# Kernel optimization log

Hardware: AMD Instinct MI355X
Metric: run time of the kernel (lower is better)

## Reference

```python
import jax, jax.numpy as jnp
import numpy as np

K = 20
EPS = 1e-5


def knn_idx(x, k):
    # x: (B,C,N); returns indices of k nearest neighbors (largest negative sq dist)
    xx = jnp.sum(x * x, axis=1)                       # (B,N)
    inner = jnp.einsum('bcn,bcm->bnm', x, x)          # (B,N,N)
    dist = 2.0 * inner - xx[:, :, None] - xx[:, None, :]
    return jax.lax.top_k(dist, k)[1]                  # (B,N,k)


def gather_nb(x, idx):
    # x: (B,C,N), idx: (B,N,k) -> (B,N,k,C)
    xt = jnp.transpose(x, (0, 2, 1))
    return jax.vmap(lambda t, i: t[i])(xt, idx)


def bn(x, g, b, m, v):
    # eval-mode batchnorm over channel axis 1
    sh = [1] * x.ndim
    sh[1] = -1
    inv = g / jnp.sqrt(v + EPS)
    return (x - m.reshape(sh)) * inv.reshape(sh) + b.reshape(sh)


def graph_feature(x, k=K):
    # x: (B,C,N) -> (B,3C,N,k): [neighbor, center, center-neighbor]
    idx = knn_idx(x, k)
    nb = gather_nb(x, idx)                            # (B,N,k,C)
    ctr = jnp.broadcast_to(jnp.transpose(x, (0, 2, 1))[:, :, None, :], nb.shape)
    f = jnp.concatenate([nb, ctr, ctr - nb], axis=-1)
    return jnp.transpose(f, (0, 3, 1, 2))


def att_pool(x, g, b, m, v, W, wb):
    # x: (B,C,N,k); BN->ReLU->1x1 conv -> softmax over k -> weighted sum
    h = jax.nn.relu(bn(x, g, b, m, v))
    act = jnp.einsum('bcnk,oc->bonk', h, W) + wb[None, :, None, None]
    scores = jax.nn.softmax(act, axis=-1)
    return jnp.sum(x * scores, axis=-1)               # (B,C,N)


def lafe(x, W1, b1, W2, b2, W3, b3):
    # local attention extraction; x: (B,3,N) -> (B,16,N)
    idx = knn_idx(x, K)
    nb = gather_nb(x, idx)                            # (B,N,k,3)
    ctr = jnp.broadcast_to(jnp.transpose(x, (0, 2, 1))[:, :, None, :], nb.shape)
    x_n = ctr - nb
    new_f = jnp.einsum('bnkc,oc->bnko', ctr, W1) + b1
    self_att = jnp.einsum('bnko,o->bnk', new_f, W3[0]) + b3[0]
    edge = jnp.einsum('bnkc,oc->bnko', x_n, W2) + b2  # (B,N,k,16)
    nb_att = jnp.einsum('bnko,o->bnk', edge, W3[0]) + b3[0]
    logits = self_att + nb_att                        # (B,N,k)
    coefs = jax.nn.softmax(jax.nn.leaky_relu(logits, 0.01), axis=-1)
    vals = jnp.einsum('bnk,bnko->bno', coefs, edge)   # (B,N,16)
    return jnp.transpose(jax.nn.elu(vals), (0, 2, 1))


def _forward(x, law1, lab1, law2, lab2, law3, lab3,
             mlp_w, mlp_b, mlp_g, mlp_be, mlp_m, mlp_v,
             c1_w, bn1_g, bn1_b, bn1_m, bn1_v,
             p1_g, p1_b, p1_m, p1_v, p1_w, p1_wb,
             c2_w, bn2_g, bn2_b, bn2_m, bn2_v,
             p2_g, p2_b, p2_m, p2_v, p2_w, p2_wb,
             c3_w, bn3_g, bn3_b, bn3_m, bn3_v):
    xm = lafe(x, law1, lab1, law2, lab2, law3, lab3)          # (B,16,N)
    x_manet = jnp.concatenate([x, xm], axis=1)                # (B,19,N)
    x_mlp = jax.nn.relu(bn(jnp.einsum('bcn,oc->bon', x_manet, mlp_w) + mlp_b[None, :, None],
                           mlp_g, mlp_be, mlp_m, mlp_v))      # (B,256,N)
    g = graph_feature(x_manet)                                # (B,57,N,k)
    h1 = jax.nn.leaky_relu(bn(jnp.einsum('bcnk,oc->bonk', g, c1_w),
                              bn1_g, bn1_b, bn1_m, bn1_v), 0.2)
    x_p1 = att_pool(h1, p1_g, p1_b, p1_m, p1_v, p1_w, p1_wb)  # (B,64,N)
    x_c1 = jnp.concatenate([x_manet, x_p1], axis=1)           # (B,83,N)
    g2 = graph_feature(x_c1)                                  # (B,249,N,k)
    h2 = jax.nn.leaky_relu(bn(jnp.einsum('bcnk,oc->bonk', g2, c2_w),
                              bn2_g, bn2_b, bn2_m, bn2_v), 0.2)
    x_p2 = att_pool(h2, p2_g, p2_b, p2_m, p2_v, p2_w, p2_wb)  # (B,256,N)
    x_c2 = jnp.concatenate([x_mlp, x_p2], axis=1)             # (B,512,N)
    return jax.nn.leaky_relu(bn(jnp.einsum('bcn,oc->bon', x_c2, c3_w),
                                bn3_g, bn3_b, bn3_m, bn3_v), 0.2)


def setup_inputs() -> dict:
    key = jax.random.key(0)
    ks = iter(jax.random.split(key, 16))
    f32 = jnp.float32
    def W(*s):
        return jax.random.normal(next(ks), s, f32) * 0.05
    B, N = 8, 2048
    def bn_params(c):
        return jnp.ones((c,), f32), jnp.zeros((c,), f32), jnp.zeros((c,), f32), jnp.ones((c,), f32)
    d = {}
    d['x'] = jax.random.normal(next(ks), (B, 3, N), f32)
    d['law1'], d['lab1'] = W(16, 3), jnp.zeros((16,), f32)
    d['law2'], d['lab2'] = W(16, 3), jnp.zeros((16,), f32)
    d['law3'], d['lab3'] = W(1, 16), jnp.zeros((1,), f32)
    d['mlp_w'], d['mlp_b'] = W(256, 19), jnp.zeros((256,), f32)
    d['mlp_g'], d['mlp_be'], d['mlp_m'], d['mlp_v'] = bn_params(256)
    d['c1_w'] = W(64, 57)
    d['bn1_g'], d['bn1_b'], d['bn1_m'], d['bn1_v'] = bn_params(64)
    d['p1_g'], d['p1_b'], d['p1_m'], d['p1_v'] = bn_params(64)
    d['p1_w'], d['p1_wb'] = W(64, 64), jnp.zeros((64,), f32)
    d['c2_w'] = W(256, 249)
    d['bn2_g'], d['bn2_b'], d['bn2_m'], d['bn2_v'] = bn_params(256)
    d['p2_g'], d['p2_b'], d['p2_m'], d['p2_v'] = bn_params(256)
    d['p2_w'], d['p2_wb'] = W(256, 256), jnp.zeros((256,), f32)
    d['c3_w'] = W(512, 512)
    d['bn3_g'], d['bn3_b'], d['bn3_m'], d['bn3_v'] = bn_params(512)
    return d


def reference(x, law1, lab1, law2, lab2, law3, lab3,
              mlp_w, mlp_b, mlp_g, mlp_be, mlp_m, mlp_v,
              c1_w, bn1_g, bn1_b, bn1_m, bn1_v,
              p1_g, p1_b, p1_m, p1_v, p1_w, p1_wb,
              c2_w, bn2_g, bn2_b, bn2_m, bn2_v,
              p2_g, p2_b, p2_m, p2_v, p2_w, p2_wb,
              c3_w, bn3_g, bn3_b, bn3_m, bn3_v):
    return _forward(x, law1, lab1, law2, lab2, law3, lab3,
                    mlp_w, mlp_b, mlp_g, mlp_be, mlp_m, mlp_v,
                    c1_w, bn1_g, bn1_b, bn1_m, bn1_v,
                    p1_g, p1_b, p1_m, p1_v, p1_w, p1_wb,
                    c2_w, bn2_g, bn2_b, bn2_m, bn2_v,
                    p2_g, p2_b, p2_m, p2_v, p2_w, p2_wb,
                    c3_w, bn3_g, bn3_b, bn3_m, bn3_v)
```

## Files before the change

kernel.cpp:

```cpp
#include <hip/hip_runtime.h>
#include <math.h>
#include <float.h>

#define NB 8
#define NP 2048
#define KNN 20
#define BN_EPS 1e-5f

typedef __attribute__((ext_vector_type(8))) short short8v;
typedef __attribute__((ext_vector_type(4))) float f32x4;
typedef __attribute__((ext_vector_type(16))) float f32x16;

__device__ __forceinline__ float leakyf(float x, float s) { return x >= 0.f ? x : s * x; }

__device__ __forceinline__ unsigned short f2bf(float f) {
  unsigned u = __float_as_uint(f);
  u = u + 0x7fffu + ((u >> 16) & 1u);
  return (unsigned short)(u >> 16);
}
__device__ __forceinline__ float bf2f(unsigned short h) {
  return __uint_as_float((unsigned)h << 16);
}
__device__ __forceinline__ unsigned sortkey(float f) {
  unsigned u = __float_as_uint(f);
  return (u & 0x80000000u) ? ~u : (u | 0x80000000u);
}

__global__ void copy_ch_k(const float* __restrict__ src, int srcC,
                          float* __restrict__ dst, int dstC, int row0, int nch) {
  int i = blockIdx.x * 256 + threadIdx.x;
  int total = NB * nch * NP;
  if (i < total) {
    int n = i & (NP - 1); int t = i >> 11; int c = t % nch; int b = t / nch;
    dst[((size_t)b * dstC + row0 + c) * NP + n] = src[((size_t)b * srcC + c) * NP + n];
  }
}

__global__ void xx_k(const float* __restrict__ src, int C, float* __restrict__ xx) {
  int i = blockIdx.x * 256 + threadIdx.x;
  if (i < NB * NP) {
    int n = i & (NP - 1); int b = i >> 11;
    const float* xb = src + (size_t)b * C * NP + n;
    float s = 0.f;
    for (int c = 0; c < C; ++c) { float v = xb[(size_t)c * NP]; s += v * v; }
    xx[i] = s;
  }
}

__global__ void prepall_k(const float* __restrict__ c1w, const float* __restrict__ mlpw,
                          const float* __restrict__ p1w, const float* __restrict__ c2w,
                          const float* __restrict__ p2w, const float* __restrict__ c3w,
                          const float* g2, const float* b2, const float* m2, const float* v2,
                          const float* pg, const float* pb, const float* pm, const float* pv,
                          const float* g3, const float* b3, const float* m3, const float* v3,
                          float* __restrict__ wn1t, float* __restrict__ wc1t,
                          float* __restrict__ mlp_wt, float* __restrict__ p1_wt,
                          unsigned short* __restrict__ Wnc, unsigned short* __restrict__ p2wB,
                          unsigned short* __restrict__ W3p,
                          float* __restrict__ fold2, float* __restrict__ fold3) {
  int i = blockIdx.x * 256 + threadIdx.x;
  if (i < 19 * 64) {
    int c = i >> 6, o = i & 63;
    float wd = c1w[o * 57 + 38 + c];
    wn1t[i] = c1w[o * 57 + c] - wd;
    wc1t[i] = c1w[o * 57 + 19 + c] + wd;
    return;
  }
  i -= 19 * 64;
  if (i < 19 * 256) {
    int o = i / 19, c = i - o * 19;
    mlp_wt[c * 256 + o] = mlpw[i];
    return;
  }
  i -= 19 * 256;
  if (i < 64 * 64) {
    int o = i >> 6, c = i & 63;
    p1_wt[c * 64 + o] = p1w[i];
    return;
  }
  i -= 64 * 64;
  if (i < 256 * 192) {
    int o = i / 192, c = i - o * 192;
    unsigned short v = 0;
    if (c < 83) v = f2bf(c2w[o * 249 + c] - c2w[o * 249 + 166 + c]);
    else if (c >= 96 && c < 96 + 83) {
      int cc = c - 96;
      v = f2bf(c2w[o * 249 + 83 + cc] + c2w[o * 249 + 166 + cc]);
    }
    Wnc[i] = v;
    return;
  }
  i -= 256 * 192;
  if (i < 256 * 256) { p2wB[i] = f2bf(p2w[i]); return; }
  i -= 256 * 256;
  if (i < 512 * 1024) {
    int o = i >> 10, k = i & 1023;
    W3p[i] = f2bf(c3w[o * 512 + (k & 511)]);
    return;
  }
  i -= 512 * 1024;
  if (i < 256) {
    int o = i;
    float s2 = g2[o] / sqrtf(v2[o] + BN_EPS);
    fold2[o] = s2; fold2[256 + o] = b2[o] - m2[o] * s2;
    float sp = pg[o] / sqrtf(pv[o] + BN_EPS);
    fold2[512 + o] = sp; fold2[768 + o] = pb[o] - pm[o] * sp;
    return;
  }
  i -= 256;
  if (i < 512) {
    int o = i;
    float s = g3[o] / sqrtf(v3[o] + BN_EPS);
    fold3[o] = s;
    fold3[512 + o] = b3[o] - m3[o] * s;
  }
}
#define PREPALL_TOTAL (19*64 + 19*256 + 64*64 + 256*192 + 256*256 + 512*1024 + 256 + 512)

__global__ void packall_k(const unsigned short* __restrict__ Wnc,
                          const unsigned short* __restrict__ p2wB,
                          unsigned short* __restrict__ pw1, unsigned short* __restrict__ pw2) {
  int i = blockIdx.x * 256 + threadIdx.x;
  if (i < 8 * 12 * 64) {
    int lane = i & 63, ks = (i >> 6) % 12, ot = i / (64 * 12);
    int o = ot * 32 + (lane & 31), c = ks * 16 + 8 * (lane >> 5);
#pragma unroll
    for (int e = 0; e < 8; ++e) pw1[i * 8 + e] = Wnc[(size_t)o * 192 + c + e];
    return;
  }
  int j = i - 8 * 12 * 64;
  if (j < 8 * 16 * 64) {
    int lane = j & 63, ks = (j >> 6) % 16, ot = j / (64 * 16);
    int o = ot * 32 + (lane & 31), c = ks * 16 + 8 * (lane >> 5);
#pragma unroll
    for (int e = 0; e < 8; ++e) pw2[j * 8 + e] = p2wB[(size_t)o * 256 + c + e];
  }
}

#define DKC 16
__global__ __launch_bounds__(256) void dist_k(const float* __restrict__ src, int C,
                                              const float* __restrict__ xx,
                                              float* __restrict__ D, int b0) {
  __shared__ float sA[DKC][64];
  __shared__ float sB[DKC][64];
  int bz = blockIdx.z; int b = b0 + bz;
  int n0 = blockIdx.x * 64, m0 = blockIdx.y * 64;
  int tid = threadIdx.x;
  int tn = tid >> 4, tm = tid & 15;
  float acc[4][4] = {};
  const float* xb = src + (size_t)b * C * NP;
  for (int k0 = 0; k0 < C; k0 += DKC) {
    for (int t = tid; t < DKC * 64; t += 256) {
      int kk = t >> 6, i = t & 63;
      int c = k0 + kk;
      float a = 0.f, bb = 0.f;
      if (c < C) { a = xb[(size_t)c * NP + n0 + i]; bb = xb[(size_t)c * NP + m0 + i]; }
      sA[kk][i] = a; sB[kk][i] = bb;
    }
    __syncthreads();
#pragma unroll
    for (int kk = 0; kk < DKC; ++kk) {
      float av[4], bv[4];
#pragma unroll
      for (int q = 0; q < 4; ++q) { av[q] = sA[kk][tn * 4 + q]; bv[q] = sB[kk][tm * 4 + q]; }
#pragma unroll
      for (int qi = 0; qi < 4; ++qi)
#pragma unroll
        for (int qj = 0; qj < 4; ++qj) acc[qi][qj] += av[qi] * bv[qj];
    }
    __syncthreads();
  }
  const float* xxb = xx + (size_t)b * NP;
#pragma unroll
  for (int qi = 0; qi < 4; ++qi) {
    int n = n0 + tn * 4 + qi; float xn = xxb[n];
    float4 dv;
    dv.x = 2.f * acc[qi][0] - xn - xxb[m0 + tm * 4 + 0];
    dv.y = 2.f * acc[qi][1] - xn - xxb[m0 + tm * 4 + 1];
    dv.z = 2.f * acc[qi][2] - xn - xxb[m0 + tm * 4 + 2];
    dv.w = 2.f * acc[qi][3] - xn - xxb[m0 + tm * 4 + 3];
    *reinterpret_cast<float4*>(&D[((size_t)bz * NP + n) * NP + m0 + tm * 4]) = dv;
  }
}

__global__ __launch_bounds__(64) void topk_k(const float* __restrict__ D,
                                             int* __restrict__ idxo, int rowbase) {
  int row = blockIdx.x;
  const float4* d4 = reinterpret_cast<const float4*>(D + (size_t)row * NP);
  int lane = threadIdx.x;
  float v[32];
#pragma unroll
  for (int j8 = 0; j8 < 8; ++j8) {
    float4 q = d4[j8 * 64 + lane];
    v[j8 * 4 + 0] = q.x; v[j8 * 4 + 1] = q.y; v[j8 * 4 + 2] = q.z; v[j8 * 4 + 3] = q.w;
  }
  int* out = idxo + (size_t)(rowbase + row) * KNN;
  for (int it = 0; it < KNN; ++it) {
    float bv = v[0]; int bj = 0;
#pragma unroll
    for (int j = 1; j < 32; ++j) { if (v[j] > bv) { bv = v[j]; bj = j; } }
    int bm = (bj >> 2) * 256 + lane * 4 + (bj & 3);
    unsigned long long key = ((unsigned long long)sortkey(bv) << 32) | (unsigned)(~bm);
#pragma unroll
    for (int off = 1; off < 64; off <<= 1) {
      unsigned long long ok = __shfl_xor(key, off);
      if (ok > key) key = ok;
    }
    int bmw = ~(unsigned)key;
    if (lane == 0) out[it] = bmw;
    if (((bmw >> 2) & 63) == lane) v[(bmw >> 8) * 4 + (bmw & 3)] = -FLT_MAX;
  }
}

__global__ __launch_bounds__(64) void lafe_k(const float* __restrict__ x, const int* __restrict__ idx,
                                             const float* __restrict__ W1, const float* __restrict__ b1,
                                             const float* __restrict__ W2, const float* __restrict__ b2,
                                             const float* __restrict__ W3, const float* __restrict__ b3,
                                             float* __restrict__ x_manet) {
  int t = blockIdx.x * 64 + threadIdx.x;
  if (t >= NB * NP) return;
  int b = t >> 11, n = t & (NP - 1);
  const float* xb = x + (size_t)b * 3 * NP;
  float ctr[3];
#pragma unroll
  for (int c = 0; c < 3; ++c) ctr[c] = xb[c * NP + n];
  float self_s = b3[0];
#pragma unroll
  for (int o = 0; o < 16; ++o) {
    float nf = b1[o];
#pragma unroll
    for (int c = 0; c < 3; ++c) nf += ctr[c] * W1[o * 3 + c];
    self_s += nf * W3[o];
  }
  const int* id = idx + (size_t)t * KNN;
  float logit[KNN];
  float mx = -FLT_MAX;
  for (int k = 0; k < KNN; ++k) {
    int j = id[k];
    float xn[3];
#pragma unroll
    for (int c = 0; c < 3; ++c) xn[c] = ctr[c] - xb[c * NP + j];
    float natt = b3[0];
#pragma unroll
    for (int o = 0; o < 16; ++o) {
      float e = b2[o];
#pragma unroll
      for (int c = 0; c < 3; ++c) e += xn[c] * W2[o * 3 + c];
      natt += e * W3[o];
    }
    float lg = self_s + natt;
    lg = leakyf(lg, 0.01f);
    logit[k] = lg; mx = fmaxf(mx, lg);
  }
  float s = 0.f;
#pragma unroll
  for (int k = 0; k < KNN; ++k) { logit[k] = expf(logit[k] - mx); s += logit[k]; }
  float invs = 1.f / s;
  float vals[16] = {};
  for (int k = 0; k < KNN; ++k) {
    int j = id[k];
    float xn[3];
#pragma unroll
    for (int c = 0; c < 3; ++c) xn[c] = ctr[c] - xb[c * NP + j];
    float w = logit[k] * invs;
#pragma unroll
    for (int o = 0; o < 16; ++o) {
      float e = b2[o];
#pragma unroll
      for (int c = 0; c < 3; ++c) e += xn[c] * W2[o * 3 + c];
      vals[o] += w * e;
    }
  }
#pragma unroll
  for (int o = 0; o < 16; ++o) {
    float v = vals[o];
    v = v > 0.f ? v : expm1f(v);
    x_manet[((size_t)b * 19 + 3 + o) * NP + n] = v;
  }
}

__global__ __launch_bounds__(256) void mlp_k(const float* __restrict__ xman, const float* __restrict__ wt,
                                             const float* __restrict__ bias,
                                             const float* __restrict__ g, const float* __restrict__ be,
                                             const float* __restrict__ m, const float* __restrict__ v,
                                             unsigned short* __restrict__ actT) {
  int o0 = (threadIdx.x & 31) * 8;
  int n = blockIdx.x * 8 + (threadIdx.x >> 5);
  int b = blockIdx.z;
  const float* xb = xman + (size_t)b * 19 * NP;
  float acc[8];
#pragma unroll
  for (int q = 0; q < 8; ++q) acc[q] = bias[o0 + q];
  for (int c = 0; c < 19; ++c) {
    float xv = xb[(size_t)c * NP + n];
    const float4* w4 = reinterpret_cast<const float4*>(wt + c * 256 + o0);
    float4 wa = w4[0], wb4 = w4[1];
    float wr[8] = {wa.x, wa.y, wa.z, wa.w, wb4.x, wb4.y, wb4.z, wb4.w};
#pragma unroll
    for (int q = 0; q < 8; ++q) acc[q] += xv * wr[q];
  }
  short8v hi8, lo8;
#pragma unroll
  for (int q = 0; q < 8; ++q) {
    int o = o0 + q;
    float inv = g[o] / sqrtf(v[o] + BN_EPS);
    float z = fmaxf((acc[q] - m[o]) * inv + be[o], 0.f);
    unsigned short h = f2bf(z);
    hi8[q] = (short)h;
    lo8[q] = (short)f2bf(z - bf2f(h));
  }
  size_t base = ((size_t)b * NP + n) * 1024;
  *reinterpret_cast<short8v*>(actT + base + o0) = hi8;
  *reinterpret_cast<short8v*>(actT + base + 512 + o0) = lo8;
}

__global__ __launch_bounds__(256) void hctr1_k(const float* __restrict__ xman,
                                               const float* __restrict__ wc1t,
                                               float* __restrict__ hctr1) {
  int o = threadIdx.x;
  int n = blockIdx.x * 4 + threadIdx.y;
  int b = blockIdx.z;
  const float* xb = xman + (size_t)b * 19 * NP + n;
  float acc = 0.f;
  for (int c = 0; c < 19; ++c) acc += wc1t[c * 64 + o] * xb[(size_t)c * NP];
  hctr1[((size_t)b * 64 + o) * NP + n] = acc;
}

__global__ __launch_bounds__(64, 1) void conv1pool_k(
    const float* __restrict__ xman, const int* __restrict__ idx,
    const float* __restrict__ wn1t, const float* __restrict__ hctr1,
    const float* __restrict__ b1g, const float* __restrict__ b1b,
    const float* __restrict__ b1m, const float* __restrict__ b1v,
    const float* __restrict__ p1g, const float* __restrict__ p1b,
    const float* __restrict__ p1m, const float* __restrict__ p1v,
    const float* __restrict__ p1wt, const float* __restrict__ p1wb,
    float* __restrict__ x_c1) {
  __shared__ __align__(16) float sg[64 * 20];
  __shared__ int jid[KNN];
  int t = blockIdx.x;
  int b = t >> 11, n = t & (NP - 1);
  int lane = threadIdx.x;
  const float* xb = xman + (size_t)b * 19 * NP;
  if (lane < KNN) jid[lane] = idx[(size_t)t * KNN + lane];
  __syncthreads();
  for (int e = lane; e < 19 * KNN; e += 64) {
    int c = e / KNN, k = e - c * KNN;
    sg[c * 20 + k] = xb[(size_t)c * NP + jid[k]];
  }
  __syncthreads();
  float hc = hctr1[((size_t)b * 64 + lane) * NP + n];
  float h[KNN];
#pragma unroll
  for (int k = 0; k < KNN; ++k) h[k] = hc;
  for (int c = 0; c < 19; ++c) {
    float wv = wn1t[c * 64 + lane];
    const float4* gp = reinterpret_cast<const float4*>(sg + c * 20);
    float4 A = gp[0], Bv = gp[1], Cv = gp[2], Dv = gp[3], E = gp[4];
    float gv[20] = {A.x,A.y,A.z,A.w,Bv.x,Bv.y,Bv.z,Bv.w,Cv.x,Cv.y,Cv.z,Cv.w,Dv.x,Dv.y,Dv.z,Dv.w,E.x,E.y,E.z,E.w};
#pragma unroll
    for (int k = 0; k < KNN; ++k) h[k] += wv * gv[k];
  }
  float inv1 = b1g[lane] / sqrtf(b1v[lane] + BN_EPS);
  float m1 = b1m[lane], bb1 = b1b[lane];
  float h1[KNN];
#pragma unroll
  for (int k = 0; k < KNN; ++k) {
    float z = (h[k] - m1) * inv1 + bb1;
    h1[k] = leakyf(z, 0.2f);
  }
  float pinv = p1g[lane] / sqrtf(p1v[lane] + BN_EPS);
  float pm = p1m[lane], pb = p1b[lane];
  __syncthreads();
#pragma unroll
  for (int k = 0; k < KNN; ++k) sg[lane * 20 + k] = fmaxf((h1[k] - pm) * pinv + pb, 0.f);
  __syncthreads();
  float act[KNN] = {};
  for (int c = 0; c < 64; ++c) {
    float wv = p1wt[c * 64 + lane];
    const float4* gp = reinterpret_cast<const float4*>(sg + c * 20);
    float4 A = gp[0], Bv = gp[1], Cv = gp[2], Dv = gp[3], E = gp[4];
    float gv[20] = {A.x,A.y,A.z,A.w,Bv.x,Bv.y,Bv.z,Bv.w,Cv.x,Cv.y,Cv.z,Cv.w,Dv.x,Dv.y,Dv.z,Dv.w,E.x,E.y,E.z,E.w};
#pragma unroll
    for (int k = 0; k < KNN; ++k) act[k] += wv * gv[k];
  }
  float wb = p1wb[lane];
  float mx = -FLT_MAX;
#pragma unroll
  for (int k = 0; k < KNN; ++k) { act[k] += wb; mx = fmaxf(mx, act[k]); }
  float s = 0.f, outv = 0.f;
#pragma unroll
  for (int k = 0; k < KNN; ++k) {
    float e = expf(act[k] - mx);
    s += e; outv += h1[k] * e;
  }
  x_c1[((size_t)b * 83 + 19 + lane) * NP + n] = outv / s;
}

__global__ __launch_bounds__(256) void t2bf_k(const float* __restrict__ xc1,
                                              unsigned short* __restrict__ xc1T) {
  __shared__ unsigned short tile[256 * 96];
  int b = blockIdx.y;
  int n0 = blockIdx.x * 256;
  int tid = threadIdx.x;
  const float* xb = xc1 + (size_t)b * 83 * NP;
  for (int c = 0; c < 83; ++c)
    tile[tid * 96 + c] = f2bf(xb[(size_t)c * NP + n0 + tid]);
#pragma unroll
  for (int c = 83; c < 96; ++c) tile[tid * 96 + c] = 0;
  __syncthreads();
  const float4* src = (const float4*)tile;
  float4* dst = (float4*)(xc1T + ((size_t)b * NP + n0) * 96);
  for (int i = tid; i < 3072; i += 256) dst[i] = src[i];
}

__global__ __launch_bounds__(256, 2) void conv2mfma_k(
    const unsigned short* __restrict__ xc1T, const int* __restrict__ idx,
    const unsigned short* __restrict__ pw1, const unsigned short* __restrict__ pw2,
    const float* __restrict__ fold, unsigned short* __restrict__ actT) {
  __shared__ unsigned short nbF[2 * 6 * 64 * 8];
  __shared__ unsigned short hhF[2 * 16 * 64 * 8];
  __shared__ int jid[64];
  int tid = threadIdx.x;
  int t0 = blockIdx.x * 2;
  int b = t0 >> 11, n0 = t0 & (NP - 1);

  if (tid < 64) {
    int p = tid >> 5, kk = tid & 31;
    int kc = kk < KNN ? kk : KNN - 1;
    jid[tid] = idx[(size_t)(t0 + p) * KNN + kc];
  }
  __syncthreads();
  for (int it = tid; it < 768; it += 256) {
    int p = it >= 384; int rem = it - p * 384;
    int kk = rem / 12, seg = rem - kk * 12;
    int j = jid[p * 32 + kk];
    short8v v = *reinterpret_cast<const short8v*>(xc1T + ((size_t)b * NP + j) * 96 + seg * 8);
    int ks = seg >> 1, hi = seg & 1;
    *reinterpret_cast<short8v*>(&nbF[(((p * 6 + ks) << 6) + hi * 32 + kk) * 8]) = v;
  }
  __syncthreads();

  int w = tid >> 6, l = tid & 63;
  int kk = l & 31, hi = l >> 5;
  int ot0 = w * 2, ot1 = w * 2 + 1;
  const short8v* pw1v = (const short8v*)pw1;
  const short8v* pw2v = (const short8v*)pw2;

  f32x16 acc[2][2];
#pragma unroll
  for (int p = 0; p < 2; ++p)
#pragma unroll
    for (int nt = 0; nt < 2; ++nt)
#pragma unroll
      for (int r = 0; r < 16; ++r) acc[p][nt][r] = 0.f;

#pragma unroll
  for (int ks = 0; ks < 6; ++ks) {
    short8v b0 = pw1v[(ot0 * 12 + ks) * 64 + l];
    short8v b1 = pw1v[(ot1 * 12 + ks) * 64 + l];
    short8v a0 = *reinterpret_cast<const short8v*>(&nbF[((ks << 6) + l) * 8]);
    short8v a1 = *reinterpret_cast<const short8v*>(&nbF[(((6 + ks) << 6) + l) * 8]);
    acc[0][0] = __builtin_amdgcn_mfma_f32_32x32x16_bf16(a0, b0, acc[0][0], 0, 0, 0);
    acc[0][1] = __builtin_amdgcn_mfma_f32_32x32x16_bf16(a0, b1, acc[0][1], 0, 0, 0);
    acc[1][0] = __builtin_amdgcn_mfma_f32_32x32x16_bf16(a1, b0, acc[1][0], 0, 0, 0);
    acc[1][1] = __builtin_amdgcn_mfma_f32_32x32x16_bf16(a1, b1, acc[1][1], 0, 0, 0);
  }
  const unsigned short* ct0 = xc1T + ((size_t)b * NP + n0) * 96 + 8 * hi;
  const unsigned short* ct1 = ct0 + 96;
#pragma unroll
  for (int ks = 0; ks < 6; ++ks) {
    short8v b0 = pw1v[(ot0 * 12 + 6 + ks) * 64 + l];
    short8v b1 = pw1v[(ot1 * 12 + 6 + ks) * 64 + l];
    short8v a0 = *reinterpret_cast<const short8v*>(ct0 + ks * 16);
    short8v a1 = *reinterpret_cast<const short8v*>(ct1 + ks * 16);
    acc[0][0] = __builtin_amdgcn_mfma_f32_32x32x16_bf16(a0, b0, acc[0][0], 0, 0, 0);
    acc[0][1] = __builtin_amdgcn_mfma_f32_32x32x16_bf16(a0, b1, acc[0][1], 0, 0, 0);
    acc[1][0] = __builtin_amdgcn_mfma_f32_32x32x16_bf16(a1, b0, acc[1][0], 0, 0, 0);
    acc[1][1] = __builtin_amdgcn_mfma_f32_32x32x16_bf16(a1, b1, acc[1][1], 0, 0, 0);
  }

#pragma unroll
  for (int p = 0; p < 2; ++p)
#pragma unroll
    for (int nt = 0; nt < 2; ++nt) {
      int o = w * 64 + nt * 32 + kk;
      float s2 = fold[o], o2 = fold[256 + o];
      float sp = fold[512 + o], op = fold[768 + o];
      int cbase = (p * 16 + (o >> 4)) * 64 + ((o >> 3) & 1) * 32;
      int s = (o >> 3) & 3;
#pragma unroll
      for (int r = 0; r < 16; ++r) {
        int row = (r & 3) + 8 * (r >> 2) + 4 * hi;
        float z = leakyf(acc[p][nt][r] * s2 + o2, 0.2f);
        acc[p][nt][r] = z;
        float hh = fmaxf(z * sp + op, 0.f);
        hhF[((cbase + row) ^ s) * 8 + (o & 7)] = f2bf(hh);
      }
    }
  __syncthreads();

  f32x16 acc2[2][2];
#pragma unroll
  for (int p = 0; p < 2; ++p)
#pragma unroll
    for (int nt = 0; nt < 2; ++nt)
#pragma unroll
      for (int r = 0; r < 16; ++r) acc2[p][nt][r] = 0.f;
#pragma unroll
  for (int ks = 0; ks < 16; ++ks) {
    int sr = (l >> 5) | ((ks & 1) << 1);
    short8v b0 = pw2v[(ot0 * 16 + ks) * 64 + l];
    short8v b1 = pw2v[(ot1 * 16 + ks) * 64 + l];
    short8v a0 = *reinterpret_cast<const short8v*>(&hhF[((((ks << 6) + l)) ^ sr) * 8]);
    short8v a1 = *reinterpret_cast<const short8v*>(&hhF[(((((16 + ks) << 6) + l)) ^ sr) * 8]);
    acc2[0][0] = __builtin_amdgcn_mfma_f32_32x32x16_bf16(a0, b0, acc2[0][0], 0, 0, 0);
    acc2[0][1] = __builtin_amdgcn_mfma_f32_32x32x16_bf16(a0, b1, acc2[0][1], 0, 0, 0);
    acc2[1][0] = __builtin_amdgcn_mfma_f32_32x32x16_bf16(a1, b0, acc2[1][0], 0, 0, 0);
    acc2[1][1] = __builtin_amdgcn_mfma_f32_32x32x16_bf16(a1, b1, acc2[1][1], 0, 0, 0);
  }

#pragma unroll
  for (int p = 0; p < 2; ++p) {
    size_t base = ((size_t)b * NP + n0 + p) * 1024;
#pragma unroll
    for (int nt = 0; nt < 2; ++nt) {
      int o = w * 64 + nt * 32 + kk;
      float mx = -FLT_MAX;
#pragma unroll
      for (int r = 0; r < 16; ++r) {
        int row = (r & 3) + 8 * (r >> 2) + 4 * hi;
        if (row < KNN) mx = fmaxf(mx, acc2[p][nt][r]);
      }
      mx = fmaxf(mx, __shfl_xor(mx, 32));
      float s = 0.f, num = 0.f;
#pragma unroll
      for (int r = 0; r < 16; ++r) {
        int row = (r & 3) + 8 * (r >> 2) + 4 * hi;
        if (row < KNN) {
          float e = __expf(acc2[p][nt][r] - mx);
          s += e; num += e * acc[p][nt][r];
        }
      }
      s += __shfl_xor(s, 32);
      num += __shfl_xor(num, 32);
      if (hi == 0) {
        float z = num / s;
        unsigned short h = f2bf(z);
        actT[base + 256 + o] = h;
        actT[base + 768 + o] = f2bf(z - bf2f(h));
      }
    }
  }
}

__global__ __launch_bounds__(256) void conv3mfma_k(const unsigned short* __restrict__ actT,
                                                   const unsigned short* __restrict__ W3p,
                                                   const float* __restrict__ fold3,
                                                   float* __restrict__ out) {
  __shared__ unsigned short sA[128 * 64];
  __shared__ unsigned short sB[128 * 64];
  int b = blockIdx.z;
  int o0 = blockIdx.x * 128, n0 = blockIdx.y * 128;
  int tid = threadIdx.x;
  int wave = tid >> 6, lane = tid & 63;
  int wr = wave >> 1, wc = wave & 1;
  int lrow = lane & 15, lkb2 = (lane >> 4) * 16, lr4 = (lane >> 4) * 4;

  f32x4 acc[4][4];
#pragma unroll
  for (int mt = 0; mt < 4; ++mt)
#pragma unroll
    for (int nt = 0; nt < 4; ++nt) acc[mt][nt] = (f32x4){0.f, 0.f, 0.f, 0.f};

  for (int k0 = 0; k0 < 1024; k0 += 64) {
    for (int i = tid; i < 2048; i += 256) {
      int half = i >> 10;
      int r = (i >> 3) & 127;
      int ci = i & 7;
      const unsigned short* src = half
          ? (actT + ((size_t)b * NP + n0 + r) * 1024 + k0 + ci * 8)
          : (W3p + (size_t)(o0 + r) * 1024 + k0 + ci * 8);
      short8v vv = *reinterpret_cast<const short8v*>(src);
      int byteoff = (r * 128 + ci * 16) ^ ((r & 7) << 4);
      *reinterpret_cast<short8v*>((char*)(half ? sB : sA) + byteoff) = vv;
    }
    __syncthreads();
#pragma unroll
    for (int ks = 0; ks < 2; ++ks) {
      short8v afr[4], bfr[4];
#pragma unroll
      for (int mt = 0; mt < 4; ++mt) {
        int r = wr * 64 + mt * 16 + lrow;
        afr[mt] = *reinterpret_cast<const short8v*>((char*)sA + ((r * 128 + ks * 64 + lkb2) ^ ((r & 7) << 4)));
      }
#pragma unroll
      for (int nt = 0; nt < 4; ++nt) {
        int r = wc * 64 + nt * 16 + lrow;
        bfr[nt] = *reinterpret_cast<const short8v*>((char*)sB + ((r * 128 + ks * 64 + lkb2) ^ ((r & 7) << 4)));
      }
#pragma unroll
      for (int mt = 0; mt < 4; ++mt)
#pragma unroll
        for (int nt = 0; nt < 4; ++nt)
          acc[mt][nt] = __builtin_amdgcn_mfma_f32_16x16x32_bf16(afr[mt], bfr[nt], acc[mt][nt], 0, 0, 0);
    }
    __syncthreads();
  }
#pragma unroll
  for (int mt = 0; mt < 4; ++mt) {
#pragma unroll
    for (int r = 0; r < 4; ++r) {
      int o = o0 + wr * 64 + mt * 16 + lr4 + r;
      float s3 = fold3[o], b3 = fold3[512 + o];
      float* op = out + ((size_t)b * 512 + o) * NP + n0 + wc * 64 + lrow;
#pragma unroll
      for (int nt = 0; nt < 4; ++nt) {
        float z = acc[mt][nt][r] * s3 + b3;
        op[nt * 16] = leakyf(z, 0.2f);
      }
    }
  }
}

extern "C" void kernel_launch(void* const* d_in, const int* in_sizes, int n_in,
                              void* d_out, int out_size, void* d_ws, size_t ws_size,
                              hipStream_t stream) {
  const float* x     = (const float*)d_in[0];
  const float* law1  = (const float*)d_in[1];
  const float* lab1  = (const float*)d_in[2];
  const float* law2  = (const float*)d_in[3];
  const float* lab2  = (const float*)d_in[4];
  const float* law3  = (const float*)d_in[5];
  const float* lab3  = (const float*)d_in[6];
  const float* mlp_w = (const float*)d_in[7];
  const float* mlp_b = (const float*)d_in[8];
  const float* mlp_g = (const float*)d_in[9];
  const float* mlp_be= (const float*)d_in[10];
  const float* mlp_m = (const float*)d_in[11];
  const float* mlp_v = (const float*)d_in[12];
  const float* c1_w  = (const float*)d_in[13];
  const float* bn1_g = (const float*)d_in[14];
  const float* bn1_b = (const float*)d_in[15];
  const float* bn1_m = (const float*)d_in[16];
  const float* bn1_v = (const float*)d_in[17];
  const float* p1_g  = (const float*)d_in[18];
  const float* p1_b  = (const float*)d_in[19];
  const float* p1_m  = (const float*)d_in[20];
  const float* p1_v  = (const float*)d_in[21];
  const float* p1_w  = (const float*)d_in[22];
  const float* p1_wb = (const float*)d_in[23];
  const float* c2_w  = (const float*)d_in[24];
  const float* bn2_g = (const float*)d_in[25];
  const float* bn2_b = (const float*)d_in[26];
  const float* bn2_m = (const float*)d_in[27];
  const float* bn2_v = (const float*)d_in[28];
  const float* p2_g  = (const float*)d_in[29];
  const float* p2_b  = (const float*)d_in[30];
  const float* p2_m  = (const float*)d_in[31];
  const float* p2_v  = (const float*)d_in[32];
  const float* p2_w  = (const float*)d_in[33];
  const float* p2_wb = (const float*)d_in[34];
  const float* c3_w  = (const float*)d_in[35];
  const float* bn3_g = (const float*)d_in[36];
  const float* bn3_b = (const float*)d_in[37];
  const float* bn3_m = (const float*)d_in[38];
  const float* bn3_v = (const float*)d_in[39];

  char* wsb = (char*)d_ws;
  size_t off = 0;
  auto alloc = [&](size_t elems) -> float* {
    float* p = (float*)(wsb + off);
    off += elems * sizeof(float);
    off = (off + 255) & ~(size_t)255;
    return p;
  };
  float* wn1t   = alloc(19 * 64);
  float* wc1t   = alloc(19 * 64);
  float* mlp_wt = alloc(19 * 256);
  float* p1_wt  = alloc(64 * 64);
  unsigned short* Wnc = (unsigned short*)alloc(256 * 192 / 2);
  unsigned short* p2wB = (unsigned short*)alloc(256 * 256 / 2);
  unsigned short* pw1 = (unsigned short*)alloc(8 * 12 * 64 * 8 / 2);
  unsigned short* pw2 = (unsigned short*)alloc(8 * 16 * 64 * 8 / 2);
  unsigned short* W3p  = (unsigned short*)alloc((size_t)512 * 1024 / 2);
  float* fold2  = alloc(1024);
  float* fold3  = alloc(1024);
  float* xxbuf  = alloc((size_t)NB * NP);
  float* x_manet= alloc((size_t)NB * 19 * NP);
  float* x_c1   = alloc((size_t)NB * 83 * NP);
  float* hctr1  = alloc((size_t)NB * 64 * NP);
  unsigned short* xc1T = (unsigned short*)alloc((size_t)NB * NP * 96 / 2);
  unsigned short* actT = (unsigned short*)alloc((size_t)NB * NP * 1024 / 2);
  int*   idxbuf = (int*)alloc((size_t)NB * NP * KNN);
  float* Dbuf   = (float*)(wsb + off);
  size_t fullD = (size_t)NB * NP * NP * sizeof(float);
  int nbc = (off + fullD <= ws_size) ? NB : 1;

  prepall_k<<<(PREPALL_TOTAL + 255) / 256, 256, 0, stream>>>(
      c1_w, mlp_w, p1_w, c2_w, p2_w, c3_w,
      bn2_g, bn2_b, bn2_m, bn2_v, p2_g, p2_b, p2_m, p2_v,
      bn3_g, bn3_b, bn3_m, bn3_v,
      wn1t, wc1t, mlp_wt, p1_wt, Wnc, p2wB, W3p, fold2, fold3);
  packall_k<<<56, 256, 0, stream>>>(Wnc, p2wB, pw1, pw2);

  auto knn = [&](const float* src, int C) {
    xx_k<<<(NB * NP + 255) / 256, 256, 0, stream>>>(src, C, xxbuf);
    for (int b0 = 0; b0 < NB; b0 += nbc) {
      dist_k<<<dim3(NP / 64, NP / 64, nbc), 256, 0, stream>>>(src, C, xxbuf, Dbuf, b0);
      topk_k<<<nbc * NP, 64, 0, stream>>>(Dbuf, idxbuf, b0 * NP);
    }
  };

  copy_ch_k<<<(NB * 3 * NP + 255) / 256, 256, 0, stream>>>(x, 3, x_manet, 19, 0, 3);

  knn(x, 3);
  lafe_k<<<(NB * NP) / 64, 64, 0, stream>>>(x, idxbuf, law1, lab1, law2, lab2, law3, lab3, x_manet);

  mlp_k<<<dim3(NP / 8, 1, NB), 256, 0, stream>>>(x_manet, mlp_wt, mlp_b, mlp_g, mlp_be, mlp_m, mlp_v, actT);

  knn(x_manet, 19);
  hctr1_k<<<dim3(NP / 4, 1, NB), dim3(64, 4), 0, stream>>>(x_manet, wc1t, hctr1);
  conv1pool_k<<<NB * NP, 64, 0, stream>>>(x_manet, idxbuf, wn1t, hctr1,
                                          bn1_g, bn1_b, bn1_m, bn1_v,
                                          p1_g, p1_b, p1_m, p1_v,
                                          p1_wt, p1_wb, x_c1);
  copy_ch_k<<<(NB * 19 * NP + 255) / 256, 256, 0, stream>>>(x_manet, 19, x_c1, 83, 0, 19);

  knn(x_c1, 83);
  t2bf_k<<<dim3(NP / 256, NB), 256, 0, stream>>>(x_c1, xc1T);
  conv2mfma_k<<<NB * NP / 2, 256, 0, stream>>>(xc1T, idxbuf, pw1, pw2, fold2, actT);

  conv3mfma_k<<<dim3(512 / 128, NP / 128, NB), 256, 0, stream>>>(actT, W3p, fold3,
                                                                 (float*)d_out);
}
```

Before: 909.4 us.

## Use point-major layouts for conv1 neighbor gather and center features; raise conv2 occupancy

Adds a transpose kernel that writes x_manet in point-major form padded to 20 floats. conv1pool can then fetch each neighbor's 19 channels with five float4 loads instead of scattered channel-strided loads, which also removes one barrier. hctr1 is now stored point-major, so conv1pool reads it contiguously. conv2mfma's launch bound goes from 2 to 3 blocks per SM, which may force register spills.

```diff
diff --git a/kernel.cpp b/kernel.cpp
--- a/kernel.cpp
+++ b/kernel.cpp
@@ -279,6 +279,21 @@
   }
 }
 
+__global__ __launch_bounds__(256) void t1f_k(const float* __restrict__ xman,
+                                             float* __restrict__ xmanT) {
+  __shared__ float tile[256 * 20];
+  int b = blockIdx.y;
+  int n0 = blockIdx.x * 256;
+  int tid = threadIdx.x;
+  const float* xb = xman + (size_t)b * 19 * NP;
+  for (int c = 0; c < 19; ++c) tile[tid * 20 + c] = xb[(size_t)c * NP + n0 + tid];
+  tile[tid * 20 + 19] = 0.f;
+  __syncthreads();
+  const float4* src = (const float4*)tile;
+  float4* dst = (float4*)(xmanT + ((size_t)b * NP + n0) * 20);
+  for (int i = tid; i < 1280; i += 256) dst[i] = src[i];
+}
+
 __global__ __launch_bounds__(256) void mlp_k(const float* __restrict__ xman, const float* __restrict__ wt,
                                              const float* __restrict__ bias,
                                              const float* __restrict__ g, const float* __restrict__ be,
@@ -316,19 +331,19 @@
 
 __global__ __launch_bounds__(256) void hctr1_k(const float* __restrict__ xman,
                                                const float* __restrict__ wc1t,
-                                               float* __restrict__ hctr1) {
+                                               float* __restrict__ hctr1T) {
   int o = threadIdx.x;
   int n = blockIdx.x * 4 + threadIdx.y;
   int b = blockIdx.z;
   const float* xb = xman + (size_t)b * 19 * NP + n;
   float acc = 0.f;
   for (int c = 0; c < 19; ++c) acc += wc1t[c * 64 + o] * xb[(size_t)c * NP];
-  hctr1[((size_t)b * 64 + o) * NP + n] = acc;
+  hctr1T[((size_t)b * NP + n) * 64 + o] = acc;
 }
 
 __global__ __launch_bounds__(64, 1) void conv1pool_k(
-    const float* __restrict__ xman, const int* __restrict__ idx,
-    const float* __restrict__ wn1t, const float* __restrict__ hctr1,
+    const float* __restrict__ xmanT, const int* __restrict__ idx,
+    const float* __restrict__ wn1t, const float* __restrict__ hctr1T,
     const float* __restrict__ b1g, const float* __restrict__ b1b,
     const float* __restrict__ b1m, const float* __restrict__ b1v,
     const float* __restrict__ p1g, const float* __restrict__ p1b,
@@ -336,19 +351,20 @@
     const float* __restrict__ p1wt, const float* __restrict__ p1wb,
     float* __restrict__ x_c1) {
   __shared__ __align__(16) float sg[64 * 20];
-  __shared__ int jid[KNN];
   int t = blockIdx.x;
   int b = t >> 11, n = t & (NP - 1);
   int lane = threadIdx.x;
-  const float* xb = xman + (size_t)b * 19 * NP;
-  if (lane < KNN) jid[lane] = idx[(size_t)t * KNN + lane];
+  if (lane < KNN) {
+    int j = idx[(size_t)t * KNN + lane];
+    const float4* src = reinterpret_cast<const float4*>(xmanT + ((size_t)b * NP + j) * 20);
+    float4 q0 = src[0], q1 = src[1], q2 = src[2], q3 = src[3], q4 = src[4];
+    float vr[20] = {q0.x,q0.y,q0.z,q0.w,q1.x,q1.y,q1.z,q1.w,q2.x,q2.y,q2.z,q2.w,
+                    q3.x,q3.y,q3.z,q3.w,q4.x,q4.y,q4.z,q4.w};
+#pragma unroll
+    for (int c = 0; c < 19; ++c) sg[c * 20 + lane] = vr[c];
+  }
   __syncthreads();
-  for (int e = lane; e < 19 * KNN; e += 64) {
-    int c = e / KNN, k = e - c * KNN;
-    sg[c * 20 + k] = xb[(size_t)c * NP + jid[k]];
-  }
-  __syncthreads();
-  float hc = hctr1[((size_t)b * 64 + lane) * NP + n];
+  float hc = hctr1T[((size_t)b * NP + n) * 64 + lane];
   float h[KNN];
 #pragma unroll
   for (int k = 0; k < KNN; ++k) h[k] = hc;
@@ -413,7 +429,7 @@
   for (int i = tid; i < 3072; i += 256) dst[i] = src[i];
 }
 
-__global__ __launch_bounds__(256, 2) void conv2mfma_k(
+__global__ __launch_bounds__(256, 3) void conv2mfma_k(
     const unsigned short* __restrict__ xc1T, const int* __restrict__ idx,
     const unsigned short* __restrict__ pw1, const unsigned short* __restrict__ pw2,
     const float* __restrict__ fold, unsigned short* __restrict__ actT) {
@@ -687,8 +703,9 @@
   float* fold3  = alloc(1024);
   float* xxbuf  = alloc((size_t)NB * NP);
   float* x_manet= alloc((size_t)NB * 19 * NP);
+  float* xmanT  = alloc((size_t)NB * NP * 20);
   float* x_c1   = alloc((size_t)NB * 83 * NP);
-  float* hctr1  = alloc((size_t)NB * 64 * NP);
+  float* hctr1T = alloc((size_t)NB * 64 * NP);
   unsigned short* xc1T = (unsigned short*)alloc((size_t)NB * NP * 96 / 2);
   unsigned short* actT = (unsigned short*)alloc((size_t)NB * NP * 1024 / 2);
   int*   idxbuf = (int*)alloc((size_t)NB * NP * KNN);
@@ -715,12 +732,13 @@
 
   knn(x, 3);
   lafe_k<<<(NB * NP) / 64, 64, 0, stream>>>(x, idxbuf, law1, lab1, law2, lab2, law3, lab3, x_manet);
+  t1f_k<<<dim3(NP / 256, NB), 256, 0, stream>>>(x_manet, xmanT);
 
   mlp_k<<<dim3(NP / 8, 1, NB), 256, 0, stream>>>(x_manet, mlp_wt, mlp_b, mlp_g, mlp_be, mlp_m, mlp_v, actT);
 
   knn(x_manet, 19);
-  hctr1_k<<<dim3(NP / 4, 1, NB), dim3(64, 4), 0, stream>>>(x_manet, wc1t, hctr1);
-  conv1pool_k<<<NB * NP, 64, 0, stream>>>(x_manet, idxbuf, wn1t, hctr1,
+  hctr1_k<<<dim3(NP / 4, 1, NB), dim3(64, 4), 0, stream>>>(x_manet, wc1t, hctr1T);
+  conv1pool_k<<<NB * NP, 64, 0, stream>>>(xmanT, idxbuf, wn1t, hctr1T,
                                           bn1_g, bn1_b, bn1_m, bn1_v,
                                           p1_g, p1_b, p1_m, p1_v,
                                           p1_wt, p1_wb, x_c1);
```

Result: faster. 889.3 us (-2.2%).
